# Optimization experiments

Measured on AMD Instinct MI355X. Metric: run time of the kernel, lower is better.

Reference implementation:

```python
import jax, jax.numpy as jnp
import numpy as np
from jax import lax

B, NPG = 128, 1024          # graphs, nodes per graph
N = B * NPG                  # total nodes
AVG_DEG = 8
E = N * AVG_DEG              # total edges
F_N, F_E = 128, 32           # node / edge feature dims
LATENT = [32, 32, 32, 1]
D = sum(LATENT)              # total_latent_dim = 97
K = 30                       # sort-pooling k
C1, C2, KW2 = 16, 32, 5      # conv1d channels / kernel
OUT = 2
DENSE = ((K - 2) // 2 + 1 - KW2 + 1) * C2  # 352


def setup_inputs() -> dict:
    key = jax.random.key(0)
    ks = jax.random.split(key, 12)
    inp = {}
    inp["node_feat"] = jax.random.normal(ks[0], (N, F_N), jnp.float32)
    inp["edge_feat"] = jax.random.normal(ks[1], (E, F_E), jnp.float32)
    inp["edge_index"] = jax.random.randint(ks[2], (2, E), 0, N)
    dims = [F_N + F_E] + LATENT
    for i in range(4):
        inp[f"W{i}"] = jax.random.normal(ks[3 + i], (dims[i], dims[i + 1]), jnp.float32) * 0.05
        inp[f"b{i}"] = jnp.zeros((dims[i + 1],), jnp.float32)
    inp["w_conv1"] = jax.random.normal(ks[7], (C1, 1, D), jnp.float32) * 0.05
    inp["b_conv1"] = jnp.zeros((C1,), jnp.float32)
    inp["w_conv2"] = jax.random.normal(ks[8], (C2, C1, KW2), jnp.float32) * 0.05
    inp["b_conv2"] = jnp.zeros((C2,), jnp.float32)
    inp["w_out"] = jax.random.normal(ks[9], (DENSE, OUT), jnp.float32) * 0.05
    inp["b_out"] = jnp.zeros((OUT,), jnp.float32)
    return inp


def _maxpool2(x):
    # MaxPool1d(2, 2) over last axis of [B, C, L]
    return lax.reduce_window(x, -jnp.inf, lax.max, (1, 1, 2), (1, 1, 2), "VALID")


def _forward(node_feat, edge_feat, W0, b0, W1, b1, W2, b2, W3, b3,
             w_conv1, b_conv1, w_conv2, b_conv2, w_out, b_out, edge_index):
    src, dst = edge_index[0], edge_index[1]
    # degree with self-loop, as in DGCNN (divide by deg after linear)
    deg = jnp.ones((N,), node_feat.dtype).at[dst].add(1.0)
    # e2npool: sum incident edge features onto destination nodes
    e2n = jax.ops.segment_sum(edge_feat, dst, num_segments=N)
    cur = jnp.concatenate([node_feat, e2n], axis=1)  # [N, F_N+F_E]
    hops = []
    for W, b in ((W0, b0), (W1, b1), (W2, b2), (W3, b3)):
        # (A + I) X  -> Linear -> / deg -> tanh
        pooled = jax.ops.segment_sum(cur[src], dst, num_segments=N) + cur
        cur = jnp.tanh((pooled @ W + b) / deg[:, None])
        hops.append(cur)
    feat = jnp.concatenate(hops, axis=1).reshape(B, NPG, D)  # [B, NPG, 97]
    # SortPooling: top-k nodes per graph by last latent channel
    _, idx = lax.top_k(feat[:, :, -1], K)                    # [B, K]
    sp = jnp.take_along_axis(feat, idx[:, :, None], axis=1)  # [B, K, D]
    x = sp.reshape(B, 1, K * D)
    x = lax.conv_general_dilated(x, w_conv1, (D,), "VALID",
                                 dimension_numbers=("NCH", "OIH", "NCH"))
    x = jax.nn.relu(x + b_conv1[None, :, None])  # [B, 16, 30]
    x = _maxpool2(x)                              # [B, 16, 15]
    x = lax.conv_general_dilated(x, w_conv2, (1,), "VALID",
                                 dimension_numbers=("NCH", "OIH", "NCH"))
    x = jax.nn.relu(x + b_conv2[None, :, None])  # [B, 32, 11]
    x = x.reshape(B, -1)                          # [B, 352]
    return jax.nn.relu(x @ w_out + b_out)         # [B, OUT]


def reference(node_feat, edge_feat, edge_index, W0, b0, W1, b1, W2, b2, W3, b3,
              w_conv1, b_conv1, w_conv2, b_conv2, w_out, b_out):
    return _forward(node_feat, edge_feat, W0, b0, W1, b1, W2, b2, W3, b3,
                    w_conv1, b_conv1, w_conv2, b_conv2, w_out, b_out, edge_index)
```

## Files before the change

kernel.cpp:

```cpp
#include <hip/hip_runtime.h>
#include <hip/hip_bf16.h>
#include <math.h>

#define N_NODES 131072
#define N_EDGES 1048576
#define B_GR    128
#define NPG_    1024
#define KTOP    30


__global__ __launch_bounds__(256) void k_zero(int* cnt) {
    int i = blockIdx.x * 256 + threadIdx.x;
    if (i < N_NODES) cnt[i] = 0;
}

__global__ __launch_bounds__(256) void k_count(const int* __restrict__ dst, int* __restrict__ cnt) {
    int e = blockIdx.x * 256 + threadIdx.x;
    if (e < N_EDGES) atomicAdd(&cnt[dst[e]], 1);
}

__global__ __launch_bounds__(256) void k_scan1(const int* __restrict__ cnt,
                                               int* __restrict__ row_start,
                                               int* __restrict__ blocksum) {
    __shared__ int s[256];
    int t = threadIdx.x;
    int i = blockIdx.x * 256 + t;
    int v = cnt[i];
    s[t] = v; __syncthreads();
    for (int o = 1; o < 256; o <<= 1) {
        int x = (t >= o) ? s[t - o] : 0;
        __syncthreads();
        s[t] += x;
        __syncthreads();
    }
    row_start[i] = s[t] - v;
    if (t == 255) blocksum[blockIdx.x] = s[t];
}

__global__ __launch_bounds__(512) void k_scan2(int* __restrict__ blocksum) {
    __shared__ int s[512];
    int t = threadIdx.x;
    int v = blocksum[t];
    s[t] = v; __syncthreads();
    for (int o = 1; o < 512; o <<= 1) {
        int x = (t >= o) ? s[t - o] : 0;
        __syncthreads();
        s[t] += x;
        __syncthreads();
    }
    blocksum[t] = s[t] - v;
}

__global__ __launch_bounds__(256) void k_scan3(int* __restrict__ row_start,
                                               const int* __restrict__ blocksum,
                                               int* __restrict__ cursor) {
    int i = blockIdx.x * 256 + threadIdx.x;
    int r = row_start[i] + blocksum[blockIdx.x];
    row_start[i] = r;
    cursor[i] = r;
}

__global__ __launch_bounds__(256) void k_fill(const int* __restrict__ src,
                                              const int* __restrict__ dst,
                                              int* __restrict__ cursor,
                                              int2* __restrict__ csr) {
    int e = blockIdx.x * 256 + threadIdx.x;
    if (e < N_EDGES) {
        int d = dst[e];
        int pos = atomicAdd(&cursor[d], 1);
        csr[pos] = make_int2(src[e], e);
    }
}


__global__ __launch_bounds__(256) void k_esum(const float* __restrict__ ef,
                                              const int* __restrict__ row_start,
                                              const int* __restrict__ cnt,
                                              const int2* __restrict__ csr,
                                              float* __restrict__ esum) {
    int g = threadIdx.x >> 5, j = threadIdx.x & 31;
    int n = blockIdx.x * 8 + g;
    int start = row_start[n], len = cnt[n];
    const int2* ce = csr + start;
    float s = 0.f;
    int i = 0;
    for (; i + 8 <= len; i += 8) {
        int e0 = ce[i].y, e1 = ce[i + 1].y, e2 = ce[i + 2].y, e3 = ce[i + 3].y;
        int e4 = ce[i + 4].y, e5 = ce[i + 5].y, e6 = ce[i + 6].y, e7 = ce[i + 7].y;
        float a0 = ef[(size_t)e0 * 32 + j], a1 = ef[(size_t)e1 * 32 + j];
        float a2 = ef[(size_t)e2 * 32 + j], a3 = ef[(size_t)e3 * 32 + j];
        float a4 = ef[(size_t)e4 * 32 + j], a5 = ef[(size_t)e5 * 32 + j];
        float a6 = ef[(size_t)e6 * 32 + j], a7 = ef[(size_t)e7 * 32 + j];
        s += ((a0 + a1) + (a2 + a3)) + ((a4 + a5) + (a6 + a7));
    }
    for (; i < len; ++i) s += ef[(size_t)ce[i].y * 32 + j];
    esum[(size_t)n * 32 + j] = s;
}


__global__ __launch_bounds__(256) void k_gemm160(const float* __restrict__ nf,
                                                 const float* __restrict__ esum,
                                                 const float* __restrict__ W0,
                                                 float* __restrict__ z0) {
    __shared__ float a[64 * 161];
    int tid = threadIdx.x;
    int n0 = blockIdx.x * 64;
    const float* nfb = nf + (size_t)n0 * 128;
    for (int f = tid; f < 8192; f += 256) {
        int n = f >> 7, k = f & 127;
        a[n * 161 + k] = nfb[f];
    }
    const float* esb = esum + (size_t)n0 * 32;
    for (int f = tid; f < 2048; f += 256) {
        int n = f >> 5, k = f & 31;
        a[n * 161 + 128 + k] = esb[f];
    }
    __syncthreads();
    int wv = __builtin_amdgcn_readfirstlane(tid >> 6);
    int lane = tid & 63;
    int c0 = wv * 8;
    float acc[8] = {0.f, 0.f, 0.f, 0.f, 0.f, 0.f, 0.f, 0.f};
    const float* ar = a + lane * 161;
    for (int k = 0; k < 160; ++k) {
        float av = ar[k];
        #pragma unroll
        for (int jj = 0; jj < 8; ++jj)
            acc[jj] += av * W0[k * 32 + c0 + jj];
    }
    float* zr = z0 + (size_t)(n0 + lane) * 32 + c0;
    *(float4*)zr = make_float4(acc[0], acc[1], acc[2], acc[3]);
    *(float4*)(zr + 4) = make_float4(acc[4], acc[5], acc[6], acc[7]);
}


__global__ __launch_bounds__(256) void k_gemm32(const float* __restrict__ h,
                                                const float* __restrict__ W,
                                                float* __restrict__ zout) {
    __shared__ float a[64 * 33];
    int tid = threadIdx.x;
    int n0 = blockIdx.x * 64;
    const float* hb = h + (size_t)n0 * 32;
    for (int f = tid; f < 2048; f += 256) {
        int n = f >> 5, k = f & 31;
        a[n * 33 + k] = hb[f];
    }
    __syncthreads();
    int wv = __builtin_amdgcn_readfirstlane(tid >> 6);
    int lane = tid & 63;
    int c0 = wv * 8;
    float acc[8] = {0.f, 0.f, 0.f, 0.f, 0.f, 0.f, 0.f, 0.f};
    const float* ar = a + lane * 33;
    #pragma unroll
    for (int k = 0; k < 32; ++k) {
        float av = ar[k];
        #pragma unroll
        for (int jj = 0; jj < 8; ++jj)
            acc[jj] += av * W[k * 32 + c0 + jj];
    }
    float* zr = zout + (size_t)(n0 + lane) * 32 + c0;
    *(float4*)zr = make_float4(acc[0], acc[1], acc[2], acc[3]);
    *(float4*)(zr + 4) = make_float4(acc[4], acc[5], acc[6], acc[7]);
}


__global__ __launch_bounds__(256) void k_g(const float* __restrict__ zin,
                                           const int* __restrict__ row_start,
                                           const int* __restrict__ cnt,
                                           const int2* __restrict__ csr,
                                           const float* __restrict__ bias,
                                           float* __restrict__ hout) {
    int g = threadIdx.x >> 5, j = threadIdx.x & 31;
    int n = blockIdx.x * 8 + g;
    int start = row_start[n], len = cnt[n];
    const int2* cs = csr + start;
    float p = zin[(size_t)n * 32 + j];
    int i = 0;
    for (; i + 8 <= len; i += 8) {
        int s0 = cs[i].x, s1 = cs[i + 1].x, s2 = cs[i + 2].x, s3 = cs[i + 3].x;
        int s4 = cs[i + 4].x, s5 = cs[i + 5].x, s6 = cs[i + 6].x, s7 = cs[i + 7].x;
        float a0 = zin[(size_t)s0 * 32 + j], a1 = zin[(size_t)s1 * 32 + j];
        float a2 = zin[(size_t)s2 * 32 + j], a3 = zin[(size_t)s3 * 32 + j];
        float a4 = zin[(size_t)s4 * 32 + j], a5 = zin[(size_t)s5 * 32 + j];
        float a6 = zin[(size_t)s6 * 32 + j], a7 = zin[(size_t)s7 * 32 + j];
        p += ((a0 + a1) + (a2 + a3)) + ((a4 + a5) + (a6 + a7));
    }
    for (; i < len; ++i) p += zin[(size_t)cs[i].x * 32 + j];
    float deg = 1.f + (float)len;
    hout[(size_t)n * 32 + j] = tanhf((p + bias[j]) / deg);
}


__global__ __launch_bounds__(256) void k_g2(const float* __restrict__ zin,
                                            const int* __restrict__ row_start,
                                            const int* __restrict__ cnt,
                                            const int2* __restrict__ csr,
                                            const float* __restrict__ bias,
                                            const float* __restrict__ W3,
                                            float* __restrict__ hout,
                                            float* __restrict__ z3) {
    int g = threadIdx.x >> 5, j = threadIdx.x & 31;
    int n = blockIdx.x * 8 + g;
    int start = row_start[n], len = cnt[n];
    const int2* cs = csr + start;
    float p = zin[(size_t)n * 32 + j];
    int i = 0;
    for (; i + 8 <= len; i += 8) {
        int s0 = cs[i].x, s1 = cs[i + 1].x, s2 = cs[i + 2].x, s3 = cs[i + 3].x;
        int s4 = cs[i + 4].x, s5 = cs[i + 5].x, s6 = cs[i + 6].x, s7 = cs[i + 7].x;
        float a0 = zin[(size_t)s0 * 32 + j], a1 = zin[(size_t)s1 * 32 + j];
        float a2 = zin[(size_t)s2 * 32 + j], a3 = zin[(size_t)s3 * 32 + j];
        float a4 = zin[(size_t)s4 * 32 + j], a5 = zin[(size_t)s5 * 32 + j];
        float a6 = zin[(size_t)s6 * 32 + j], a7 = zin[(size_t)s7 * 32 + j];
        p += ((a0 + a1) + (a2 + a3)) + ((a4 + a5) + (a6 + a7));
    }
    for (; i < len; ++i) p += zin[(size_t)cs[i].x * 32 + j];
    float deg = 1.f + (float)len;
    float h = tanhf((p + bias[j]) / deg);
    hout[(size_t)n * 32 + j] = h;
    float t = h * W3[j];
    #pragma unroll
    for (int o = 16; o; o >>= 1) t += __shfl_xor(t, o, 32);
    if (j == 0) z3[n] = t;
}


__global__ __launch_bounds__(256) void k_g3(const float* __restrict__ z3,
                                            const int* __restrict__ row_start,
                                            const int* __restrict__ cnt,
                                            const int2* __restrict__ csr,
                                            const float* __restrict__ b3,
                                            float* __restrict__ val) {
    int n = blockIdx.x * 256 + threadIdx.x;
    int start = row_start[n], len = cnt[n];
    const int2* cs = csr + start;
    float s = z3[n];
    int i = 0;
    for (; i + 4 <= len; i += 4)
        s += z3[cs[i].x] + z3[cs[i + 1].x] + z3[cs[i + 2].x] + z3[cs[i + 3].x];
    for (; i < len; ++i) s += z3[cs[i].x];
    float deg = 1.f + (float)len;
    val[n] = tanhf((s + b3[0]) / deg);
}


__global__ __launch_bounds__(256) void k_head(const float* __restrict__ h0,
                                              const float* __restrict__ h1,
                                              const float* __restrict__ h2,
                                              const float* __restrict__ val,
                                              const float* __restrict__ wc1,
                                              const float* __restrict__ bc1,
                                              const float* __restrict__ wc2,
                                              const float* __restrict__ bc2,
                                              const float* __restrict__ wout,
                                              const float* __restrict__ bout,
                                              float* __restrict__ out) {
    __shared__ float vals[1024];
    __shared__ int selidx[KTOP];
    __shared__ float sp[KTOP * 97];
    __shared__ float y1[16 * 30];
    __shared__ float pool[16 * 15];
    __shared__ float y2[352];
    int b = blockIdx.x, tid = threadIdx.x;
    const float* vb = val + (size_t)b * NPG_;
    for (int u = tid; u < NPG_; u += 256) vals[u] = vb[u];
    __syncthreads();
    if (tid < 64) {
        unsigned long long keys[16];
        #pragma unroll
        for (int r = 0; r < 16; ++r) {
            int u = tid * 16 + r;
            unsigned int bb = __float_as_uint(vals[u]);
            unsigned int ord = (bb & 0x80000000u) ? ~bb : (bb | 0x80000000u);
            keys[r] = ((unsigned long long)ord << 32) |
                      (unsigned long long)(0xFFFFFFFFu - (unsigned int)u);
        }
        for (int k = 0; k < KTOP; ++k) {
            unsigned long long m = keys[0];
            #pragma unroll
            for (int r = 1; r < 16; ++r) m = (keys[r] > m) ? keys[r] : m;
            #pragma unroll
            for (int o = 32; o; o >>= 1) {
                unsigned long long t = __shfl_xor(m, o);
                m = (t > m) ? t : m;
            }
            int u = (int)(0xFFFFFFFFu - (unsigned int)(m & 0xFFFFFFFFull));
            if (tid == 0) selidx[k] = u;
            #pragma unroll
            for (int r = 0; r < 16; ++r)
                if (tid * 16 + r == u) keys[r] = 0ull;
        }
    }
    __syncthreads();
    size_t nb = (size_t)b * NPG_;
    for (int idx = tid; idx < KTOP * 32; idx += 256) {
        int t = idx >> 5, d = idx & 31;
        size_t s = (nb + (size_t)selidx[t]) * 32;
        sp[t * 97 + d]      = h0[s + d];
        sp[t * 97 + 32 + d] = h1[s + d];
        sp[t * 97 + 64 + d] = h2[s + d];
    }
    if (tid < KTOP) sp[tid * 97 + 96] = vb[selidx[tid]];
    __syncthreads();
    for (int idx = tid; idx < 480; idx += 256) {
        int t = idx >> 4, c = idx & 15;
        float acc = bc1[c];
        for (int d = 0; d < 97; ++d) acc += sp[t * 97 + d] * wc1[c * 97 + d];
        y1[c * 30 + t] = fmaxf(acc, 0.f);
    }
    __syncthreads();
    for (int idx = tid; idx < 240; idx += 256) {
        int c = idx / 15, u = idx - c * 15;
        pool[c * 15 + u] = fmaxf(y1[c * 30 + 2 * u], y1[c * 30 + 2 * u + 1]);
    }
    __syncthreads();
    for (int idx = tid; idx < 352; idx += 256) {
        int o = idx / 11, t = idx - o * 11;
        float acc = bc2[o];
        for (int i = 0; i < 16; ++i)
            for (int kk = 0; kk < 5; ++kk)
                acc += pool[i * 15 + t + kk] * wc2[(o * 16 + i) * 5 + kk];
        y2[idx] = fmaxf(acc, 0.f);
    }
    __syncthreads();
    if (tid < 2) {
        float acc = bout[tid];
        for (int m = 0; m < 352; ++m) acc += y2[m] * wout[m * 2 + tid];
        out[b * 2 + tid] = fmaxf(acc, 0.f);
    }
}


extern "C" void kernel_launch(void* const* d_in, const int* in_sizes, int n_in,
                              void* d_out, int out_size, void* d_ws, size_t ws_size,
                              hipStream_t stream) {
    const float* node_feat = (const float*)d_in[0];
    const float* edge_feat = (const float*)d_in[1];
    const int*   eidx      = (const int*)d_in[2];
    const float* W0 = (const float*)d_in[3];
    const float* b0 = (const float*)d_in[4];
    const float* W1 = (const float*)d_in[5];
    const float* b1 = (const float*)d_in[6];
    const float* W2 = (const float*)d_in[7];
    const float* b2 = (const float*)d_in[8];
    const float* W3 = (const float*)d_in[9];
    const float* b3 = (const float*)d_in[10];
    const float* wc1 = (const float*)d_in[11];
    const float* bc1 = (const float*)d_in[12];
    const float* wc2 = (const float*)d_in[13];
    const float* bc2 = (const float*)d_in[14];
    const float* wout = (const float*)d_in[15];
    const float* bout = (const float*)d_in[16];
    float* out = (float*)d_out;

    const int* src = eidx;
    const int* dst = eidx + N_EDGES;

    char* ws = (char*)d_ws;
    size_t off = 0;
    auto alloc = [&](size_t bytes) -> char* {
        char* p = ws + off;
        off += (bytes + 255) & ~(size_t)255;
        return p;
    };
    int* cnt       = (int*)alloc((size_t)N_NODES * 4);
    int* row_start = (int*)alloc((size_t)N_NODES * 4);
    int* cursor    = (int*)alloc((size_t)N_NODES * 4);
    int* blocksum  = (int*)alloc(512 * 4);
    int2* csr      = (int2*)alloc((size_t)N_EDGES * 8);
    float* esum    = (float*)alloc((size_t)N_NODES * 32 * 4);
    float* z0      = (float*)alloc((size_t)N_NODES * 32 * 4);
    float* z1      = (float*)alloc((size_t)N_NODES * 32 * 4);
    float* z2      = (float*)alloc((size_t)N_NODES * 32 * 4);
    float* h0      = (float*)alloc((size_t)N_NODES * 32 * 4);
    float* h1      = (float*)alloc((size_t)N_NODES * 32 * 4);
    float* h2      = (float*)alloc((size_t)N_NODES * 32 * 4);
    float* z3      = (float*)alloc((size_t)N_NODES * 4);
    float* val     = (float*)alloc((size_t)N_NODES * 4);
    (void)ws_size;

    k_zero<<<N_NODES / 256, 256, 0, stream>>>(cnt);
    k_count<<<N_EDGES / 256, 256, 0, stream>>>(dst, cnt);
    k_scan1<<<N_NODES / 256, 256, 0, stream>>>(cnt, row_start, blocksum);
    k_scan2<<<1, 512, 0, stream>>>(blocksum);
    k_scan3<<<N_NODES / 256, 256, 0, stream>>>(row_start, blocksum, cursor);
    k_fill<<<N_EDGES / 256, 256, 0, stream>>>(src, dst, cursor, csr);
    k_esum<<<N_NODES / 8, 256, 0, stream>>>(edge_feat, row_start, cnt, csr, esum);
    k_gemm160<<<N_NODES / 64, 256, 0, stream>>>(node_feat, esum, W0, z0);
    k_g<<<N_NODES / 8, 256, 0, stream>>>(z0, row_start, cnt, csr, b0, h0);
    k_gemm32<<<N_NODES / 64, 256, 0, stream>>>(h0, W1, z1);
    k_g<<<N_NODES / 8, 256, 0, stream>>>(z1, row_start, cnt, csr, b1, h1);
    k_gemm32<<<N_NODES / 64, 256, 0, stream>>>(h1, W2, z2);
    k_g2<<<N_NODES / 8, 256, 0, stream>>>(z2, row_start, cnt, csr, b2, W3, h2, z3);
    k_g3<<<N_NODES / 256, 256, 0, stream>>>(z3, row_start, cnt, csr, b3, val);
    k_head<<<B_GR, 256, 0, stream>>>(h0, h1, h2, val, wc1, bc1, wc2, bc2, wout, bout, out);
}
```

Before: 670.1 us.

## Fuse neighbor aggregation with next-layer GEMM and batch four nodes per warp

Measured after the change: 598.5 us. 1.12x faster.

```diff
diff --git a/kernel.cpp b/kernel.cpp
--- a/kernel.cpp
+++ b/kernel.cpp
@@ -79,22 +79,37 @@
                                               const int2* __restrict__ csr,
                                               float* __restrict__ esum) {
     int g = threadIdx.x >> 5, j = threadIdx.x & 31;
-    int n = blockIdx.x * 8 + g;
-    int start = row_start[n], len = cnt[n];
-    const int2* ce = csr + start;
-    float s = 0.f;
-    int i = 0;
-    for (; i + 8 <= len; i += 8) {
-        int e0 = ce[i].y, e1 = ce[i + 1].y, e2 = ce[i + 2].y, e3 = ce[i + 3].y;
-        int e4 = ce[i + 4].y, e5 = ce[i + 5].y, e6 = ce[i + 6].y, e7 = ce[i + 7].y;
-        float a0 = ef[(size_t)e0 * 32 + j], a1 = ef[(size_t)e1 * 32 + j];
-        float a2 = ef[(size_t)e2 * 32 + j], a3 = ef[(size_t)e3 * 32 + j];
-        float a4 = ef[(size_t)e4 * 32 + j], a5 = ef[(size_t)e5 * 32 + j];
-        float a6 = ef[(size_t)e6 * 32 + j], a7 = ef[(size_t)e7 * 32 + j];
-        s += ((a0 + a1) + (a2 + a3)) + ((a4 + a5) + (a6 + a7));
-    }
-    for (; i < len; ++i) s += ef[(size_t)ce[i].y * 32 + j];
-    esum[(size_t)n * 32 + j] = s;
+    int n0 = (blockIdx.x * 8 + g) * 4;
+    int st[4], ln[4];
+    #pragma unroll
+    for (int i = 0; i < 4; ++i) { st[i] = row_start[n0 + i]; ln[i] = cnt[n0 + i]; }
+    float acc[4] = {0.f, 0.f, 0.f, 0.f};
+    int base = 0;
+    while ((ln[0] > base) | (ln[1] > base) | (ln[2] > base) | (ln[3] > base)) {
+        int eid[4][8];
+        #pragma unroll
+        for (int i = 0; i < 4; ++i) {
+            #pragma unroll
+            for (int s = 0; s < 8; ++s) {
+                int idx = base + s;
+                int a = st[i] + ((idx < ln[i]) ? idx : 0);
+                a = (a < N_EDGES) ? a : 0;
+                eid[i][s] = csr[a].y;
+            }
+        }
+        #pragma unroll
+        for (int i = 0; i < 4; ++i) {
+            #pragma unroll
+            for (int s = 0; s < 8; ++s) {
+                float v = ef[(size_t)eid[i][s] * 32 + j];
+                acc[i] += ((base + s) < ln[i]) ? v : 0.f;
+            }
+        }
+        base += 8;
+    }
+    #pragma unroll
+    for (int i = 0; i < 4; ++i)
+        esum[(size_t)(n0 + i) * 32 + j] = acc[i];
 }
 
 
@@ -133,94 +148,121 @@
 }
 
 
-__global__ __launch_bounds__(256) void k_gemm32(const float* __restrict__ h,
-                                                const float* __restrict__ W,
-                                                float* __restrict__ zout) {
-    __shared__ float a[64 * 33];
+__global__ __launch_bounds__(256) void k_layer(const float* __restrict__ zin,
+                                               const int* __restrict__ row_start,
+                                               const int* __restrict__ cnt,
+                                               const int2* __restrict__ csr,
+                                               const float* __restrict__ bias,
+                                               const float* __restrict__ Wn,
+                                               float* __restrict__ hout,
+                                               float* __restrict__ znext) {
+    __shared__ float Ws[1024];
     int tid = threadIdx.x;
-    int n0 = blockIdx.x * 64;
-    const float* hb = h + (size_t)n0 * 32;
-    for (int f = tid; f < 2048; f += 256) {
-        int n = f >> 5, k = f & 31;
-        a[n * 33 + k] = hb[f];
-    }
-    __syncthreads();
-    int wv = __builtin_amdgcn_readfirstlane(tid >> 6);
-    int lane = tid & 63;
-    int c0 = wv * 8;
-    float acc[8] = {0.f, 0.f, 0.f, 0.f, 0.f, 0.f, 0.f, 0.f};
-    const float* ar = a + lane * 33;
-    #pragma unroll
+    for (int f = tid; f < 1024; f += 256) Ws[f] = Wn[f];
+    __syncthreads();
+    int g = tid >> 5, j = tid & 31;
+    int n0 = (blockIdx.x * 8 + g) * 4;
+    int st[4], ln[4];
+    #pragma unroll
+    for (int i = 0; i < 4; ++i) { st[i] = row_start[n0 + i]; ln[i] = cnt[n0 + i]; }
+    float acc[4];
+    #pragma unroll
+    for (int i = 0; i < 4; ++i) acc[i] = zin[(size_t)(n0 + i) * 32 + j];
+    int base = 0;
+    while ((ln[0] > base) | (ln[1] > base) | (ln[2] > base) | (ln[3] > base)) {
+        int sid[4][8];
+        #pragma unroll
+        for (int i = 0; i < 4; ++i) {
+            #pragma unroll
+            for (int s = 0; s < 8; ++s) {
+                int idx = base + s;
+                int a = st[i] + ((idx < ln[i]) ? idx : 0);
+                a = (a < N_EDGES) ? a : 0;
+                sid[i][s] = csr[a].x;
+            }
+        }
+        #pragma unroll
+        for (int i = 0; i < 4; ++i) {
+            #pragma unroll
+            for (int s = 0; s < 8; ++s) {
+                float v = zin[(size_t)sid[i][s] * 32 + j];
+                acc[i] += ((base + s) < ln[i]) ? v : 0.f;
+            }
+        }
+        base += 8;
+    }
+    float bj = bias[j];
+    float h[4];
+    #pragma unroll
+    for (int i = 0; i < 4; ++i) {
+        float deg = 1.f + (float)ln[i];
+        h[i] = tanhf((acc[i] + bj) / deg);
+        hout[(size_t)(n0 + i) * 32 + j] = h[i];
+    }
+    float z[4] = {0.f, 0.f, 0.f, 0.f};
     for (int k = 0; k < 32; ++k) {
-        float av = ar[k];
-        #pragma unroll
-        for (int jj = 0; jj < 8; ++jj)
-            acc[jj] += av * W[k * 32 + c0 + jj];
-    }
-    float* zr = zout + (size_t)(n0 + lane) * 32 + c0;
-    *(float4*)zr = make_float4(acc[0], acc[1], acc[2], acc[3]);
-    *(float4*)(zr + 4) = make_float4(acc[4], acc[5], acc[6], acc[7]);
-}
-
-
-__global__ __launch_bounds__(256) void k_g(const float* __restrict__ zin,
-                                           const int* __restrict__ row_start,
-                                           const int* __restrict__ cnt,
-                                           const int2* __restrict__ csr,
-                                           const float* __restrict__ bias,
-                                           float* __restrict__ hout) {
+        float w = Ws[k * 32 + j];
+        #pragma unroll
+        for (int i = 0; i < 4; ++i)
+            z[i] += __shfl(h[i], k, 32) * w;
+    }
+    #pragma unroll
+    for (int i = 0; i < 4; ++i)
+        znext[(size_t)(n0 + i) * 32 + j] = z[i];
+}
+
+
+__global__ __launch_bounds__(256) void k_layer3(const float* __restrict__ zin,
+                                                const int* __restrict__ row_start,
+                                                const int* __restrict__ cnt,
+                                                const int2* __restrict__ csr,
+                                                const float* __restrict__ bias,
+                                                const float* __restrict__ W3,
+                                                float* __restrict__ hout,
+                                                float* __restrict__ z3) {
     int g = threadIdx.x >> 5, j = threadIdx.x & 31;
-    int n = blockIdx.x * 8 + g;
-    int start = row_start[n], len = cnt[n];
-    const int2* cs = csr + start;
-    float p = zin[(size_t)n * 32 + j];
-    int i = 0;
-    for (; i + 8 <= len; i += 8) {
-        int s0 = cs[i].x, s1 = cs[i + 1].x, s2 = cs[i + 2].x, s3 = cs[i + 3].x;
-        int s4 = cs[i + 4].x, s5 = cs[i + 5].x, s6 = cs[i + 6].x, s7 = cs[i + 7].x;
-        float a0 = zin[(size_t)s0 * 32 + j], a1 = zin[(size_t)s1 * 32 + j];
-        float a2 = zin[(size_t)s2 * 32 + j], a3 = zin[(size_t)s3 * 32 + j];
-        float a4 = zin[(size_t)s4 * 32 + j], a5 = zin[(size_t)s5 * 32 + j];
-        float a6 = zin[(size_t)s6 * 32 + j], a7 = zin[(size_t)s7 * 32 + j];
-        p += ((a0 + a1) + (a2 + a3)) + ((a4 + a5) + (a6 + a7));
-    }
-    for (; i < len; ++i) p += zin[(size_t)cs[i].x * 32 + j];
-    float deg = 1.f + (float)len;
-    hout[(size_t)n * 32 + j] = tanhf((p + bias[j]) / deg);
-}
-
-
-__global__ __launch_bounds__(256) void k_g2(const float* __restrict__ zin,
-                                            const int* __restrict__ row_start,
-                                            const int* __restrict__ cnt,
-                                            const int2* __restrict__ csr,
-                                            const float* __restrict__ bias,
-                                            const float* __restrict__ W3,
-                                            float* __restrict__ hout,
-                                            float* __restrict__ z3) {
-    int g = threadIdx.x >> 5, j = threadIdx.x & 31;
-    int n = blockIdx.x * 8 + g;
-    int start = row_start[n], len = cnt[n];
-    const int2* cs = csr + start;
-    float p = zin[(size_t)n * 32 + j];
-    int i = 0;
-    for (; i + 8 <= len; i += 8) {
-        int s0 = cs[i].x, s1 = cs[i + 1].x, s2 = cs[i + 2].x, s3 = cs[i + 3].x;
-        int s4 = cs[i + 4].x, s5 = cs[i + 5].x, s6 = cs[i + 6].x, s7 = cs[i + 7].x;
-        float a0 = zin[(size_t)s0 * 32 + j], a1 = zin[(size_t)s1 * 32 + j];
-        float a2 = zin[(size_t)s2 * 32 + j], a3 = zin[(size_t)s3 * 32 + j];
-        float a4 = zin[(size_t)s4 * 32 + j], a5 = zin[(size_t)s5 * 32 + j];
-        float a6 = zin[(size_t)s6 * 32 + j], a7 = zin[(size_t)s7 * 32 + j];
-        p += ((a0 + a1) + (a2 + a3)) + ((a4 + a5) + (a6 + a7));
-    }
-    for (; i < len; ++i) p += zin[(size_t)cs[i].x * 32 + j];
-    float deg = 1.f + (float)len;
-    float h = tanhf((p + bias[j]) / deg);
-    hout[(size_t)n * 32 + j] = h;
-    float t = h * W3[j];
-    #pragma unroll
-    for (int o = 16; o; o >>= 1) t += __shfl_xor(t, o, 32);
-    if (j == 0) z3[n] = t;
+    int n0 = (blockIdx.x * 8 + g) * 4;
+    int st[4], ln[4];
+    #pragma unroll
+    for (int i = 0; i < 4; ++i) { st[i] = row_start[n0 + i]; ln[i] = cnt[n0 + i]; }
+    float acc[4];
+    #pragma unroll
+    for (int i = 0; i < 4; ++i) acc[i] = zin[(size_t)(n0 + i) * 32 + j];
+    int base = 0;
+    while ((ln[0] > base) | (ln[1] > base) | (ln[2] > base) | (ln[3] > base)) {
+        int sid[4][8];
+        #pragma unroll
+        for (int i = 0; i < 4; ++i) {
+            #pragma unroll
+            for (int s = 0; s < 8; ++s) {
+                int idx = base + s;
+                int a = st[i] + ((idx < ln[i]) ? idx : 0);
+                a = (a < N_EDGES) ? a : 0;
+                sid[i][s] = csr[a].x;
+            }
+        }
+        #pragma unroll
+        for (int i = 0; i < 4; ++i) {
+            #pragma unroll
+            for (int s = 0; s < 8; ++s) {
+                float v = zin[(size_t)sid[i][s] * 32 + j];
+                acc[i] += ((base + s) < ln[i]) ? v : 0.f;
+            }
+        }
+        base += 8;
+    }
+    float bj = bias[j];
+    float w3 = W3[j];
+    #pragma unroll
+    for (int i = 0; i < 4; ++i) {
+        float deg = 1.f + (float)ln[i];
+        float h = tanhf((acc[i] + bj) / deg);
+        hout[(size_t)(n0 + i) * 32 + j] = h;
+        float t = h * w3;
+        #pragma unroll
+        for (int o = 16; o; o >>= 1) t += __shfl_xor(t, o, 32);
+        if (j == 0) z3[n0 + i] = t;
+    }
 }
 
 
@@ -384,13 +426,11 @@
     k_scan2<<<1, 512, 0, stream>>>(blocksum);
     k_scan3<<<N_NODES / 256, 256, 0, stream>>>(row_start, blocksum, cursor);
     k_fill<<<N_EDGES / 256, 256, 0, stream>>>(src, dst, cursor, csr);
-    k_esum<<<N_NODES / 8, 256, 0, stream>>>(edge_feat, row_start, cnt, csr, esum);
+    k_esum<<<N_NODES / 32, 256, 0, stream>>>(edge_feat, row_start, cnt, csr, esum);
     k_gemm160<<<N_NODES / 64, 256, 0, stream>>>(node_feat, esum, W0, z0);
-    k_g<<<N_NODES / 8, 256, 0, stream>>>(z0, row_start, cnt, csr, b0, h0);
-    k_gemm32<<<N_NODES / 64, 256, 0, stream>>>(h0, W1, z1);
-    k_g<<<N_NODES / 8, 256, 0, stream>>>(z1, row_start, cnt, csr, b1, h1);
-    k_gemm32<<<N_NODES / 64, 256, 0, stream>>>(h1, W2, z2);
-    k_g2<<<N_NODES / 8, 256, 0, stream>>>(z2, row_start, cnt, csr, b2, W3, h2, z3);
+    k_layer<<<N_NODES / 32, 256, 0, stream>>>(z0, row_start, cnt, csr, b0, W1, h0, z1);
+    k_layer<<<N_NODES / 32, 256, 0, stream>>>(z1, row_start, cnt, csr, b1, W2, h1, z2);
+    k_layer3<<<N_NODES / 32, 256, 0, stream>>>(z2, row_start, cnt, csr, b2, W3, h2, z3);
     k_g3<<<N_NODES / 256, 256, 0, stream>>>(z3, row_start, cnt, csr, b3, val);
     k_head<<<B_GR, 256, 0, stream>>>(h0, h1, h2, val, wc1, bc1, wc2, bc2, wout, bout, out);
 }
```
